# Performance work log

Hardware: AMD Instinct MI355X
Metric: run time of the kernel (lower is better)

## Reference

```python
import jax, jax.numpy as jnp
import numpy as np

TEMPERATURE = 0.1
LISTWISE_W = 1.0
HARD_NEG_K = 32
MARGIN = 0.5
PAIRWISE_W = 0.5
NEG = jnp.float32(-1e30)  # finite stand-in for -inf (avoids inf-inf NaNs)


def _masked_segment_lse(vals, mask, idx, num_segments):
    """Stable segment-wise logsumexp over vals where mask is True."""
    v = jnp.where(mask, vals, NEG)
    m = jax.ops.segment_max(v, idx, num_segments=num_segments)  # [G]
    ex = jnp.where(mask, jnp.exp(vals - m[idx]), 0.0)
    s = jax.ops.segment_sum(ex, idx, num_segments=num_segments)
    tiny = jnp.finfo(vals.dtype).tiny
    return m + jnp.log(jnp.maximum(s, tiny))


def setup_inputs() -> dict:
    key = jax.random.key(0)
    k1, k2 = jax.random.split(key)
    G, L = 4096, 512  # graphs x edges-per-graph
    E = G * L
    logits = jax.random.normal(k1, (E,), dtype=jnp.float32)
    targets = (jax.random.uniform(k2, (E,)) < 0.1).astype(jnp.float32)
    edge_batch = jnp.repeat(jnp.arange(G, dtype=jnp.int32), L)  # sorted segment ids
    return {"logits": logits, "targets": targets, "edge_batch": edge_batch, "num_graphs": G}


def reference(logits, targets, edge_batch, num_graphs):
    G = int(num_graphs)
    E = logits.shape[0]
    L = E // G  # equal-size segments by construction

    # ---- listwise term ----
    scaled = logits / TEMPERATURE
    all_mask = jnp.ones_like(logits, dtype=bool)
    log_denom = _masked_segment_lse(scaled, all_mask, edge_batch, G)
    # (every graph has edges here, so the has_edge zeroing in torch is a no-op)
    pos_mask = targets > 0.5
    log_num = _masked_segment_lse(scaled, pos_mask, edge_batch, G)
    pos_cnt = jax.ops.segment_sum(pos_mask.astype(jnp.float32), edge_batch, num_segments=G)
    has_pos = pos_cnt > 0
    log_num_safe = jnp.where(has_pos, log_num, log_denom)
    listwise_den = jnp.maximum(jnp.sum(has_pos.astype(jnp.float32)), 1.0)
    listwise = jnp.sum(-(log_num_safe - log_denom)) / listwise_den

    # ---- pairwise hard-negative term ----
    k = HARD_NEG_K
    lg = logits.reshape(G, L)
    pos2 = (targets > 0.5).reshape(G, L)
    neg_vals = jnp.where(pos2, NEG, lg)
    hard, _ = jax.lax.top_k(neg_vals, k)  # [G, k], descending
    neg_cnt = jnp.sum(~pos2, axis=1)
    kg = jnp.minimum(neg_cnt, k)  # per-graph k = min(hard_neg_k, #neg)
    valid_n = jnp.arange(k)[None, :] < kg[:, None]  # [G, k]
    hard = jnp.where(valid_n, hard, NEG)
    # softplus(margin + z_n - z_p) over pos p x top-k negatives n: [G, L, k]
    pair = jax.nn.softplus(MARGIN + hard[:, None, :] - lg[:, :, None])
    pm = pos2[:, :, None] & valid_n[:, None, :]
    psum = jnp.sum(jnp.where(pm, pair, 0.0), axis=(1, 2))  # [G]
    Pg = jnp.sum(pos2, axis=1).astype(jnp.float32)
    kgf = kg.astype(jnp.float32)
    active = (Pg > 0) & (kgf > 0)
    contrib = jnp.where(active, psum / jnp.maximum(Pg * kgf, 1.0), 0.0)
    n_pg = jnp.sum(active.astype(jnp.float32))
    pairwise = jnp.sum(contrib) / jnp.maximum(n_pg, 1.0)

    return LISTWISE_W * listwise + PAIRWISE_W * pairwise
```

## Files before the change

### kernel.cpp

```cpp
#include <hip/hip_runtime.h>
#include <math.h>

#define L        512
#define BLK      256
#define WPB      4
#define KTOP     32
#define NEGV     (-1e30f)

#define LOG2E    1.4426950408889634f
#define LOG2E10  14.426950408889634f
#define LN2      0.6931471805599453f
#define M_L2E    0.7213475204444817f

#if __has_builtin(__builtin_amdgcn_exp2f)
#define EXP2F(x) __builtin_amdgcn_exp2f(x)
#else
#define EXP2F(x) exp2f(x)
#endif
#if __has_builtin(__builtin_amdgcn_logf)
#define LOG2F(x) __builtin_amdgcn_logf(x)
#else
#define LOG2F(x) __log2f(x)
#endif

__device__ __forceinline__ float softplus_l2(float x2) {
    return fmaxf(x2, 0.0f) + LOG2F(1.0f + EXP2F(fminf(x2, -x2)));
}

__device__ __forceinline__ float waveSum(float v) {
#pragma unroll
    for (int off = 32; off; off >>= 1)
        v += __shfl_xor(v, off, 64);
    return v;
}

__device__ __forceinline__ unsigned lanes_below(unsigned long long m) {
    return __builtin_amdgcn_mbcnt_hi((unsigned)(m >> 32),
           __builtin_amdgcn_mbcnt_lo((unsigned)(m & 0xffffffffull), 0u));
}

__global__ __launch_bounds__(BLK) void graph_loss_kernel(
    const float* __restrict__ logits,
    const float* __restrict__ targets,
    int G,
    float* __restrict__ partials )
{
    __shared__ float hard_s[WPB][KTOP];
    __shared__ float pos_s[WPB][L];
    __shared__ float wres[WPB][4];

    const int tid  = threadIdx.x;
    const int lane = tid & 63;
    const int w    = tid >> 6;
    const int g    = blockIdx.x * WPB + w;
    const bool valid = (g < G);

    float lw = 0.0f, contrib = 0.0f;
    float has_pos_f = 0.0f, active_f = 0.0f;

    if (valid) {
        const float4* lg4 = (const float4*)(logits  + (size_t)g * L);
        const float4* tg4 = (const float4*)(targets + (size_t)g * L);
        const float4 la = lg4[lane * 2], lb = lg4[lane * 2 + 1];
        const float4 ta = tg4[lane * 2], tb = tg4[lane * 2 + 1];
        float v[8]  = {la.x, la.y, la.z, la.w, lb.x, lb.y, lb.z, lb.w};
        float tv[8] = {ta.x, ta.y, ta.z, ta.w, tb.x, tb.y, tb.z, tb.w};
        bool  p[8];
        unsigned nu[8];

#pragma unroll
        for (int e = 0; e < 8; e++) {
            p[e] = tv[e] > 0.5f;
            const unsigned i = __float_as_uint(v[e]);
            const unsigned msk = (unsigned)((int)i >> 31) | 0x80000000u;
            nu[e] = p[e] ? 0u : (i ^ msk);
        }

        float u[8];
        float s_mx = NEGV, p_mx = NEGV;
#pragma unroll
        for (int e = 0; e < 8; e++) {
            u[e] = v[e] * LOG2E10;
            s_mx = fmaxf(s_mx, u[e]);
            p_mx = fmaxf(p_mx, p[e] ? u[e] : NEGV);
        }
#pragma unroll
        for (int off = 32; off; off >>= 1) {
            s_mx = fmaxf(s_mx, __shfl_xor(s_mx, off, 64));
            p_mx = fmaxf(p_mx, __shfl_xor(p_mx, off, 64));
        }
        float se_all = 0.0f, se_pos = 0.0f;
#pragma unroll
        for (int e = 0; e < 8; e++) {
            se_all += EXP2F(u[e] - s_mx);
            const float ep = EXP2F(u[e] - p_mx);
            se_pos += p[e] ? ep : 0.0f;
        }
#pragma unroll
        for (int off = 32; off; off >>= 1) {
            se_all += __shfl_xor(se_all, off, 64);
            se_pos += __shfl_xor(se_pos, off, 64);
        }

        int pbase = 0;
#pragma unroll
        for (int e = 0; e < 8; e++) {
            const unsigned long long m = __ballot((int)p[e]);
            if (p[e]) pos_s[w][pbase + lanes_below(m)] = v[e] * LOG2E;
            pbase += __popcll(m);
        }
        const int P = pbase;

        if (P > 0) {
            has_pos_f = 1.0f;
            lw = LN2 * ((s_mx + LOG2F(se_all)) - (p_mx + LOG2F(se_pos)));
        }
        const int neg_cnt = L - P;
        const int K = neg_cnt < KTOP ? neg_cnt : KTOP;
        const bool do_pair = (P > 0) && (K > 0);

        if (do_pair) {
            unsigned prefix = 0u;
            int exact = 0;
            for (int b = 31; b >= 0; --b) {
                const unsigned cand = prefix | (1u << b);
                int cnt = 0;
#pragma unroll
                for (int e = 0; e < 8; e++)
                    cnt += __popcll(__ballot(nu[e] >= cand));
                if (cnt >= K) {
                    prefix = cand;
                    if (cnt == K) { exact = 1; break; }
                }
            }
            const unsigned lo = prefix - (unsigned)exact;
            const unsigned ti = prefix ^ ((prefix & 0x80000000u) ? 0x80000000u
                                                                 : 0xFFFFFFFFu);
            const float tval = __uint_as_float(ti);

            int hbase = 0;
#pragma unroll
            for (int e = 0; e < 8; e++) {
                const bool gt = nu[e] > lo;
                const unsigned long long m = __ballot((int)gt);
                if (gt) hard_s[w][hbase + lanes_below(m)] = v[e];
                hbase += __popcll(m);
            }
            const int c_gt = hbase;

            float psum2 = 0.0f;
            for (int n = 0; n < c_gt; n++) {
                const float c2 = fmaf(hard_s[w][n], LOG2E, M_L2E);
                for (int pp = lane; pp < P; pp += 64)
                    psum2 += softplus_l2(c2 - pos_s[w][pp]);
            }
            const float wt = (float)(K - c_gt);
            if (wt > 0.0f) {
                const float c2 = fmaf(tval, LOG2E, M_L2E);
                float tsum = 0.0f;
                for (int pp = lane; pp < P; pp += 64)
                    tsum += softplus_l2(c2 - pos_s[w][pp]);
                psum2 += wt * tsum;
            }
            const float psum = waveSum(psum2) * LN2;
            contrib  = psum / fmaxf((float)P * (float)K, 1.0f);
            active_f = 1.0f;
        }
    }

    if (lane == 0) {
        wres[w][0] = lw;
        wres[w][1] = has_pos_f;
        wres[w][2] = contrib;
        wres[w][3] = active_f;
    }
    __syncthreads();
    if (tid < 4) {
        partials[blockIdx.x * 4 + tid] =
            wres[0][tid] + wres[1][tid] + wres[2][tid] + wres[3][tid];
    }
}

__global__ __launch_bounds__(BLK) void finalize_kernel(
    const float* __restrict__ partials, int nblocks, float* __restrict__ out)
{
    float s0 = 0, s1 = 0, s2 = 0, s3 = 0;
    for (int i = threadIdx.x; i < nblocks; i += BLK) {
        const float4 p = ((const float4*)partials)[i];
        s0 += p.x; s1 += p.y; s2 += p.z; s3 += p.w;
    }
#pragma unroll
    for (int off = 32; off; off >>= 1) {
        s0 += __shfl_xor(s0, off, 64);
        s1 += __shfl_xor(s1, off, 64);
        s2 += __shfl_xor(s2, off, 64);
        s3 += __shfl_xor(s3, off, 64);
    }
    __shared__ float red[4][4];
    const int lane = threadIdx.x & 63, wid = threadIdx.x >> 6;
    if (lane == 0) { red[wid][0]=s0; red[wid][1]=s1; red[wid][2]=s2; red[wid][3]=s3; }
    __syncthreads();
    if (threadIdx.x == 0) {
        const float a0 = red[0][0]+red[1][0]+red[2][0]+red[3][0];
        const float a1 = red[0][1]+red[1][1]+red[2][1]+red[3][1];
        const float a2 = red[0][2]+red[1][2]+red[2][2]+red[3][2];
        const float a3 = red[0][3]+red[1][3]+red[2][3]+red[3][3];
        const float listwise = a0 / fmaxf(a1, 1.0f);
        const float pairwise = a2 / fmaxf(a3, 1.0f);
        out[0] = 1.0f * listwise + 0.5f * pairwise;
    }
}

extern "C" void kernel_launch(void* const* d_in, const int* in_sizes, int n_in,
                              void* d_out, int out_size, void* d_ws, size_t ws_size,
                              hipStream_t stream) {
    const float* logits  = (const float*)d_in[0];
    const float* targets = (const float*)d_in[1];
    const int E = in_sizes[0];
    const int G = E / L;
    const int nblocks = (G + WPB - 1) / WPB;

    float* partials = (float*)d_ws;
    graph_loss_kernel<<<nblocks, BLK, 0, stream>>>(logits, targets, G, partials);
    finalize_kernel<<<1, BLK, 0, stream>>>(partials, nblocks, (float*)d_out);
}
```

Baseline: 83.77 us.

## Use one-wave blocks per graph and restructure pairwise loop with lane-shuffled negatives

Each block now holds a single 64-lane wave that handles one graph, which removes the block-level __syncthreads and the shared-memory partial reduction, and each block writes a float4 partial. The listwise term now reuses the global max for both sums, dropping the second max reduction and exp. In the common K==32 case the pairwise loop gives each lane one positive, broadcasts the 32 hard negatives with shuffles, and uses four accumulators. This replaces the serial per-negative loop that read LDS on every iteration. The risks are more blocks to schedule and possible underflow in se_pos when all positives sit far below the global max.

```diff
diff --git a/kernel.cpp b/kernel.cpp
--- a/kernel.cpp
+++ b/kernel.cpp
@@ -2,8 +2,7 @@
 #include <math.h>
 
 #define L        512
-#define BLK      256
-#define WPB      4
+#define BLK      64
 #define KTOP     32
 #define NEGV     (-1e30f)
 
@@ -27,13 +26,6 @@
     return fmaxf(x2, 0.0f) + LOG2F(1.0f + EXP2F(fminf(x2, -x2)));
 }
 
-__device__ __forceinline__ float waveSum(float v) {
-#pragma unroll
-    for (int off = 32; off; off >>= 1)
-        v += __shfl_xor(v, off, 64);
-    return v;
-}
-
 __device__ __forceinline__ unsigned lanes_below(unsigned long long m) {
     return __builtin_amdgcn_mbcnt_hi((unsigned)(m >> 32),
            __builtin_amdgcn_mbcnt_lo((unsigned)(m & 0xffffffffull), 0u));
@@ -42,151 +34,147 @@
 __global__ __launch_bounds__(BLK) void graph_loss_kernel(
     const float* __restrict__ logits,
     const float* __restrict__ targets,
-    int G,
-    float* __restrict__ partials )
+    float4* __restrict__ partials )
 {
-    __shared__ float hard_s[WPB][KTOP];
-    __shared__ float pos_s[WPB][L];
-    __shared__ float wres[WPB][4];
-
-    const int tid  = threadIdx.x;
-    const int lane = tid & 63;
-    const int w    = tid >> 6;
-    const int g    = blockIdx.x * WPB + w;
-    const bool valid = (g < G);
-
-    float lw = 0.0f, contrib = 0.0f;
-    float has_pos_f = 0.0f, active_f = 0.0f;
-
-    if (valid) {
-        const float4* lg4 = (const float4*)(logits  + (size_t)g * L);
-        const float4* tg4 = (const float4*)(targets + (size_t)g * L);
-        const float4 la = lg4[lane * 2], lb = lg4[lane * 2 + 1];
-        const float4 ta = tg4[lane * 2], tb = tg4[lane * 2 + 1];
-        float v[8]  = {la.x, la.y, la.z, la.w, lb.x, lb.y, lb.z, lb.w};
-        float tv[8] = {ta.x, ta.y, ta.z, ta.w, tb.x, tb.y, tb.z, tb.w};
-        bool  p[8];
-        unsigned nu[8];
-
+    __shared__ float pos_s[L];
+    __shared__ float hard_s[KTOP];
+
+    const int lane = threadIdx.x;
+    const int g    = blockIdx.x;
+
+    const float4* lg4 = (const float4*)(logits  + (size_t)g * L);
+    const float4* tg4 = (const float4*)(targets + (size_t)g * L);
+    const float4 la = lg4[lane * 2], lb = lg4[lane * 2 + 1];
+    const float4 ta = tg4[lane * 2], tb = tg4[lane * 2 + 1];
+    float v[8]  = {la.x, la.y, la.z, la.w, lb.x, lb.y, lb.z, lb.w};
+    float tv[8] = {ta.x, ta.y, ta.z, ta.w, tb.x, tb.y, tb.z, tb.w};
+    bool  p[8];
+    unsigned nu[8];
+
+#pragma unroll
+    for (int e = 0; e < 8; e++) {
+        p[e] = tv[e] > 0.5f;
+        const unsigned i = __float_as_uint(v[e]);
+        const unsigned msk = (unsigned)((int)i >> 31) | 0x80000000u;
+        nu[e] = p[e] ? 0u : (i ^ msk);
+    }
+
+    int pbase = 0;
+#pragma unroll
+    for (int e = 0; e < 8; e++) {
+        const unsigned long long m = __ballot((int)p[e]);
+        if (p[e]) pos_s[pbase + lanes_below(m)] = v[e] * LOG2E;
+        pbase += __popcll(m);
+    }
+    const int P = pbase;
+
+    float u[8];
+    float s_mx = NEGV;
+#pragma unroll
+    for (int e = 0; e < 8; e++) {
+        u[e] = v[e] * LOG2E10;
+        s_mx = fmaxf(s_mx, u[e]);
+    }
+#pragma unroll
+    for (int off = 32; off; off >>= 1)
+        s_mx = fmaxf(s_mx, __shfl_xor(s_mx, off, 64));
+
+    float se_all = 0.0f, se_pos = 0.0f;
+#pragma unroll
+    for (int e = 0; e < 8; e++) {
+        const float ep = EXP2F(u[e] - s_mx);
+        se_all += ep;
+        se_pos += p[e] ? ep : 0.0f;
+    }
+#pragma unroll
+    for (int off = 32; off; off >>= 1) {
+        se_all += __shfl_xor(se_all, off, 64);
+        se_pos += __shfl_xor(se_pos, off, 64);
+    }
+
+    float lw = 0.0f, contrib = 0.0f, hp = 0.0f, act = 0.0f;
+    if (P > 0) {
+        hp = 1.0f;
+        lw = LN2 * (LOG2F(se_all) - LOG2F(se_pos));
+    }
+    const int neg_cnt = L - P;
+    const int K = neg_cnt < KTOP ? neg_cnt : KTOP;
+
+    if (P > 0 && K > 0) {
+        unsigned prefix = 0u;
+        int exact = 0;
+        for (int b = 31; b >= 0; --b) {
+            const unsigned cand = prefix | (1u << b);
+            int cnt = 0;
+#pragma unroll
+            for (int e = 0; e < 8; e++)
+                cnt += __popcll(__ballot(nu[e] >= cand));
+            if (cnt >= K) {
+                prefix = cand;
+                if (cnt == K) { exact = 1; break; }
+            }
+        }
+        const unsigned lo = prefix - (unsigned)exact;
+        const unsigned ti = prefix ^ ((prefix & 0x80000000u) ? 0x80000000u
+                                                             : 0xFFFFFFFFu);
+        const float tval = __uint_as_float(ti);
+        const float tc2  = fmaf(tval, LOG2E, M_L2E);
+
+        int hbase = 0;
 #pragma unroll
         for (int e = 0; e < 8; e++) {
-            p[e] = tv[e] > 0.5f;
-            const unsigned i = __float_as_uint(v[e]);
-            const unsigned msk = (unsigned)((int)i >> 31) | 0x80000000u;
-            nu[e] = p[e] ? 0u : (i ^ msk);
+            const bool gt = nu[e] > lo;
+            const unsigned long long m = __ballot((int)gt);
+            if (gt) hard_s[hbase + lanes_below(m)] = fmaf(v[e], LOG2E, M_L2E);
+            hbase += __popcll(m);
         }
-
-        float u[8];
-        float s_mx = NEGV, p_mx = NEGV;
-#pragma unroll
-        for (int e = 0; e < 8; e++) {
-            u[e] = v[e] * LOG2E10;
-            s_mx = fmaxf(s_mx, u[e]);
-            p_mx = fmaxf(p_mx, p[e] ? u[e] : NEGV);
+        const int c_gt = hbase;
+
+        float psum = 0.0f;
+        if (K == KTOP) {
+            const float hc = (lane < c_gt) ? hard_s[lane & (KTOP - 1)] : tc2;
+            for (int base = 0; base < P; base += 64) {
+                const float qs = pos_s[base + lane];
+                float a0 = 0.0f, a1 = 0.0f, a2 = 0.0f, a3 = 0.0f;
+#pragma unroll
+                for (int n = 0; n < KTOP; n += 4) {
+                    a0 += softplus_l2(__shfl(hc, n + 0, 64) - qs);
+                    a1 += softplus_l2(__shfl(hc, n + 1, 64) - qs);
+                    a2 += softplus_l2(__shfl(hc, n + 2, 64) - qs);
+                    a3 += softplus_l2(__shfl(hc, n + 3, 64) - qs);
+                }
+                const float s = (a0 + a1) + (a2 + a3);
+                psum += (base + lane < P) ? s : 0.0f;
+            }
+        } else {
+            for (int n = 0; n < c_gt; n++) {
+                const float c2 = hard_s[n];
+                for (int pp = lane; pp < P; pp += 64)
+                    psum += softplus_l2(c2 - pos_s[pp]);
+            }
+            if (K > c_gt) {
+                float t = 0.0f;
+                for (int pp = lane; pp < P; pp += 64)
+                    t += softplus_l2(tc2 - pos_s[pp]);
+                psum += (float)(K - c_gt) * t;
+            }
         }
 #pragma unroll
-        for (int off = 32; off; off >>= 1) {
-            s_mx = fmaxf(s_mx, __shfl_xor(s_mx, off, 64));
-            p_mx = fmaxf(p_mx, __shfl_xor(p_mx, off, 64));
-        }
-        float se_all = 0.0f, se_pos = 0.0f;
-#pragma unroll
-        for (int e = 0; e < 8; e++) {
-            se_all += EXP2F(u[e] - s_mx);
-            const float ep = EXP2F(u[e] - p_mx);
-            se_pos += p[e] ? ep : 0.0f;
-        }
-#pragma unroll
-        for (int off = 32; off; off >>= 1) {
-            se_all += __shfl_xor(se_all, off, 64);
-            se_pos += __shfl_xor(se_pos, off, 64);
-        }
-
-        int pbase = 0;
-#pragma unroll
-        for (int e = 0; e < 8; e++) {
-            const unsigned long long m = __ballot((int)p[e]);
-            if (p[e]) pos_s[w][pbase + lanes_below(m)] = v[e] * LOG2E;
-            pbase += __popcll(m);
-        }
-        const int P = pbase;
-
-        if (P > 0) {
-            has_pos_f = 1.0f;
-            lw = LN2 * ((s_mx + LOG2F(se_all)) - (p_mx + LOG2F(se_pos)));
-        }
-        const int neg_cnt = L - P;
-        const int K = neg_cnt < KTOP ? neg_cnt : KTOP;
-        const bool do_pair = (P > 0) && (K > 0);
-
-        if (do_pair) {
-            unsigned prefix = 0u;
-            int exact = 0;
-            for (int b = 31; b >= 0; --b) {
-                const unsigned cand = prefix | (1u << b);
-                int cnt = 0;
-#pragma unroll
-                for (int e = 0; e < 8; e++)
-                    cnt += __popcll(__ballot(nu[e] >= cand));
-                if (cnt >= K) {
-                    prefix = cand;
-                    if (cnt == K) { exact = 1; break; }
-                }
-            }
-            const unsigned lo = prefix - (unsigned)exact;
-            const unsigned ti = prefix ^ ((prefix & 0x80000000u) ? 0x80000000u
-                                                                 : 0xFFFFFFFFu);
-            const float tval = __uint_as_float(ti);
-
-            int hbase = 0;
-#pragma unroll
-            for (int e = 0; e < 8; e++) {
-                const bool gt = nu[e] > lo;
-                const unsigned long long m = __ballot((int)gt);
-                if (gt) hard_s[w][hbase + lanes_below(m)] = v[e];
-                hbase += __popcll(m);
-            }
-            const int c_gt = hbase;
-
-            float psum2 = 0.0f;
-            for (int n = 0; n < c_gt; n++) {
-                const float c2 = fmaf(hard_s[w][n], LOG2E, M_L2E);
-                for (int pp = lane; pp < P; pp += 64)
-                    psum2 += softplus_l2(c2 - pos_s[w][pp]);
-            }
-            const float wt = (float)(K - c_gt);
-            if (wt > 0.0f) {
-                const float c2 = fmaf(tval, LOG2E, M_L2E);
-                float tsum = 0.0f;
-                for (int pp = lane; pp < P; pp += 64)
-                    tsum += softplus_l2(c2 - pos_s[w][pp]);
-                psum2 += wt * tsum;
-            }
-            const float psum = waveSum(psum2) * LN2;
-            contrib  = psum / fmaxf((float)P * (float)K, 1.0f);
-            active_f = 1.0f;
-        }
-    }
-
-    if (lane == 0) {
-        wres[w][0] = lw;
-        wres[w][1] = has_pos_f;
-        wres[w][2] = contrib;
-        wres[w][3] = active_f;
-    }
-    __syncthreads();
-    if (tid < 4) {
-        partials[blockIdx.x * 4 + tid] =
-            wres[0][tid] + wres[1][tid] + wres[2][tid] + wres[3][tid];
-    }
-}
-
-__global__ __launch_bounds__(BLK) void finalize_kernel(
-    const float* __restrict__ partials, int nblocks, float* __restrict__ out)
+        for (int off = 32; off; off >>= 1)
+            psum += __shfl_xor(psum, off, 64);
+        contrib = LN2 * psum / fmaxf((float)P * (float)K, 1.0f);
+        act = 1.0f;
+    }
+
+    if (lane == 0) partials[g] = make_float4(lw, hp, contrib, act);
+}
+
+__global__ __launch_bounds__(256) void finalize_kernel(
+    const float4* __restrict__ partials, int n, float* __restrict__ out)
 {
     float s0 = 0, s1 = 0, s2 = 0, s3 = 0;
-    for (int i = threadIdx.x; i < nblocks; i += BLK) {
-        const float4 p = ((const float4*)partials)[i];
+    for (int i = threadIdx.x; i < n; i += 256) {
+        const float4 p = partials[i];
         s0 += p.x; s1 += p.y; s2 += p.z; s3 += p.w;
     }
 #pragma unroll
@@ -218,9 +206,8 @@
     const float* targets = (const float*)d_in[1];
     const int E = in_sizes[0];
     const int G = E / L;
-    const int nblocks = (G + WPB - 1) / WPB;
-
-    float* partials = (float*)d_ws;
-    graph_loss_kernel<<<nblocks, BLK, 0, stream>>>(logits, targets, G, partials);
-    finalize_kernel<<<1, BLK, 0, stream>>>(partials, nblocks, (float*)d_out);
-}
+
+    float4* partials = (float4*)d_ws;
+    graph_loss_kernel<<<G, BLK, 0, stream>>>(logits, targets, partials);
+    finalize_kernel<<<1, 256, 0, stream>>>(partials, G, (float*)d_out);
+}
```

Result: slower. 88.22 us (+5.3%).
